# Performance work log

Hardware: AMD Instinct MI355X
Metric: run time of the kernel (lower is better)

The kernel has to match this reference:

```python
import jax, jax.numpy as jnp
import numpy as np
from jax import lax

B, T, P, H, O = 64, 96, 256, 128, 24  # batch, seq_len, num_points, hidden_dim, pred_len


def setup_inputs() -> dict:
    key = jax.random.key(0)
    ks = jax.random.split(key, 7)
    s = 1.0 / np.sqrt(H)  # torch LSTM/Linear default init scale
    return {
        "x": jax.random.normal(ks[0], (B, T, P, 1), dtype=jnp.float32),
        "W_ih": jax.random.uniform(ks[1], (P, 4 * H, 1), jnp.float32, -s, s),
        "W_hh": jax.random.uniform(ks[2], (P, 4 * H, H), jnp.float32, -s, s),
        "b_ih": jax.random.uniform(ks[3], (P, 4 * H), jnp.float32, -s, s),
        "b_hh": jax.random.uniform(ks[4], (P, 4 * H), jnp.float32, -s, s),
        "W_fc": jax.random.uniform(ks[5], (P, O, H), jnp.float32, -s, s),
        "b_fc": jax.random.uniform(ks[6], (P, O), jnp.float32, -s, s),
    }


def reference(x, W_ih, W_hh, b_ih, b_hh, W_fc, b_fc):
    # x: [B, T, P, F]; model uses only feature 0
    xs = x[..., 0]  # [B, T, P]
    # input_dim == 1, so input-to-gate contribution is a scaled broadcast of W_ih
    # precompute for all timesteps: [T, B, P, 4H]
    gx = jnp.einsum("btp,pg->tbpg", xs, W_ih[:, :, 0]) + (b_ih + b_hh)

    def step(carry, gxt):
        h, c = carry  # [B, P, H] each
        gates = gxt + jnp.einsum("bph,pgh->bpg", h, W_hh)  # [B, P, 4H]
        i, f, g, o = jnp.split(gates, 4, axis=-1)  # torch gate order i,f,g,o
        i = jax.nn.sigmoid(i)
        f = jax.nn.sigmoid(f)
        g = jnp.tanh(g)
        o = jax.nn.sigmoid(o)
        c = f * c + i * g
        h = o * jnp.tanh(c)
        return (h, c), None

    h0 = jnp.zeros((B, P, H), dtype=x.dtype)
    (h, _), _ = lax.scan(step, (h0, h0), gx)
    # per-point Linear on final hidden state: [B, P, O]
    out = jnp.einsum("bph,poh->bpo", h, W_fc) + b_fc
    # original stacks point outputs on last dim -> [B, pred_len, P]
    return jnp.transpose(out, (0, 2, 1))
```

## Files before the change

kernel.cpp:

```cpp
#include <hip/hip_runtime.h>
#include <hip/hip_bf16.h>

#define Bdim 64
#define Tdim 96
#define Pdim 256
#define Hdim 128
#define Gdim 512
#define Odim 24
#define BH   32

typedef _Float16 f16x8 __attribute__((ext_vector_type(8)));
typedef float    f32x16 __attribute__((ext_vector_type(16)));
typedef float    f32x2  __attribute__((ext_vector_type(2)));

union H8 { uint4 u4; unsigned short s[8]; _Float16 h[8]; f16x8 v; };
union HS { _Float16 h; unsigned short s; };

__device__ __forceinline__ float exp2_fast(float x) {
#if __has_builtin(__builtin_amdgcn_exp2f)
    return __builtin_amdgcn_exp2f(x);
#else
    return __expf(x * 0.6931471805599453f);
#endif
}

__global__ __launch_bounds__(1024, 4)
void lstm_fused(const float* __restrict__ x,
                const float* __restrict__ W_ih,
                const float* __restrict__ W_hh,
                const float* __restrict__ b_ih,
                const float* __restrict__ b_hh,
                const float* __restrict__ W_fc,
                const float* __restrict__ b_fc,
                float* __restrict__ out)
{
    __shared__ alignas(16) unsigned short hb0[2][BH * Hdim];
    __shared__ alignas(16) unsigned short hb1[2][BH * Hdim];

    const int p   = blockIdx.x;
    const int tid = threadIdx.x;
    const int w   = tid >> 6;
    const int l31 = tid & 31;
    const int hi  = (tid >> 5) & 1;

    const float L1 = 1.4426950408889634f;
    const float L2 = 2.0f * L1;

    for (int i = tid; i < 2 * BH * Hdim; i += 1024) ((unsigned short*)hb0)[i] = 0;
    for (int i = tid; i < 2 * BH * Hdim; i += 1024) ((unsigned short*)hb1)[i] = 0;

    f16x8 afr[9];
    {
        const int rp   = w * 32 + l31;
        const int u    = l31 >> 2;
        const int kl   = ((u & 1) << 2) | (u >> 1);
        const int orow = ((rp & 3) << 7) | (w * 8 + kl);
        const float sc = ((rp & 3) == 2) ? L2 : L1;
        const float* rowp = W_hh + (size_t)p * Gdim * Hdim + (size_t)orow * Hdim;
        #pragma unroll
        for (int ks = 0; ks < 8; ++ks) {
            int k0 = ks * 16 + hi * 8;
            float4 va = *(const float4*)(rowp + k0);
            float4 vb = *(const float4*)(rowp + k0 + 4);
            H8 u8;
            u8.h[0] = (_Float16)(sc * va.x); u8.h[1] = (_Float16)(sc * va.y);
            u8.h[2] = (_Float16)(sc * va.z); u8.h[3] = (_Float16)(sc * va.w);
            u8.h[4] = (_Float16)(sc * vb.x); u8.h[5] = (_Float16)(sc * vb.y);
            u8.h[6] = (_Float16)(sc * vb.z); u8.h[7] = (_Float16)(sc * vb.w);
            afr[ks] = u8.v;
        }
        H8 u9;
        #pragma unroll
        for (int j = 0; j < 8; ++j) u9.s[j] = 0;
        if (hi == 0) {
            u9.h[0] = (_Float16)(sc * W_ih[(size_t)p * Gdim + orow]);
            u9.h[1] = (_Float16)(sc * (b_ih[(size_t)p * Gdim + orow] +
                                       b_hh[(size_t)p * Gdim + orow]));
        }
        afr[8] = u9.v;
    }

    auto ldh = [&](const unsigned short* hb, int ks) -> H8 {
        H8 r;
        int c   = ks * 2 + hi;
        int off = (l31 << 8) + ((c ^ (l31 & 15)) << 4);
        r.u4 = *(const uint4*)((const char*)hb + off);
        return r;
    };

    auto ep_pair = [&](const f32x16& a, int j, f32x2* cr) -> unsigned {
        f32x2 yi = {a[8 * j + 0], a[8 * j + 4]};
        f32x2 yf = {a[8 * j + 1], a[8 * j + 5]};
        f32x2 yg = {a[8 * j + 2], a[8 * j + 6]};
        f32x2 yo = {a[8 * j + 3], a[8 * j + 7]};
        f32x2 Ef = {exp2_fast(-yf.x), exp2_fast(-yf.y)};
        f32x2 Ei = {exp2_fast(-yi.x), exp2_fast(-yi.y)};
        f32x2 Eg = {exp2_fast(yg.x),  exp2_fast(yg.y)};
        f32x2 t1 = Ef + 1.0f;
        f32x2 t2 = Ei + 1.0f;
        f32x2 t3 = Eg + 1.0f;
        f32x2 t4 = Eg - 1.0f;
        f32x2 den = (t1 * t2) * t3;
        f32x2 num = (cr[j] * t2) * t3 + (L2 * t4) * t1;
        float D = den.x * den.y;
        float r = __builtin_amdgcn_rcpf(D);
        f32x2 inv = {r * den.y, r * den.x};
        f32x2 cn  = num * inv;
        cn.x = __builtin_amdgcn_fmed3f(cn.x, -30.0f, 30.0f);
        cn.y = __builtin_amdgcn_fmed3f(cn.y, -30.0f, 30.0f);
        cr[j] = cn;
        f32x2 Eo = {exp2_fast(-yo.x), exp2_fast(-yo.y)};
        f32x2 Ec = {exp2_fast(cn.x),  exp2_fast(cn.y)};
        f32x2 d2 = (Eo + 1.0f) * (Ec + 1.0f);
        float D2 = d2.x * d2.y;
        float r2 = __builtin_amdgcn_rcpf(D2);
        f32x2 j2 = {r2 * d2.y, r2 * d2.x};
        f32x2 hv = (Ec - 1.0f) * j2;
        HS ha; ha.h = (_Float16)hv.x;
        HS hc; hc.h = (_Float16)hv.y;
        return (unsigned)ha.s | ((unsigned)hc.s << 16);
    };

    auto ep_write = [&](unsigned lo, unsigned hi2, unsigned short* wb) {
        int base = (l31 << 7) + ((w ^ (l31 & 15)) << 3) + (hi << 2);
        uint2 v; v.x = lo; v.y = hi2;
        *(uint2*)(wb + base) = v;
    };

    auto phase = [&](const unsigned short* rb, unsigned short* wb,
                     f32x16& acc, const f32x16& ar, f32x2* cr, float xv,
                     bool doGemm, bool doEp) {
        if (doGemm) {
            f32x16 z;
            #pragma unroll
            for (int j = 0; j < 16; ++j) z[j] = 0.f;
            H8 bg;
            #pragma unroll
            for (int j = 0; j < 8; ++j) bg.s[j] = 0;
            if (hi == 0) { bg.h[0] = (_Float16)xv; bg.h[1] = (_Float16)1.0f; }
            acc = __builtin_amdgcn_mfma_f32_32x32x16_f16(afr[8], bg.v, z, 0, 0, 0);
            H8 f0 = ldh(rb, 0), f1 = ldh(rb, 1);
            H8 f2 = ldh(rb, 2), f3 = ldh(rb, 3);
            acc = __builtin_amdgcn_mfma_f32_32x32x16_f16(afr[0], f0.v, acc, 0, 0, 0);
            acc = __builtin_amdgcn_mfma_f32_32x32x16_f16(afr[1], f1.v, acc, 0, 0, 0);
            unsigned e0 = 0;
            if (doEp) e0 = ep_pair(ar, 0, cr);
            H8 f4 = ldh(rb, 4), f5 = ldh(rb, 5);
            acc = __builtin_amdgcn_mfma_f32_32x32x16_f16(afr[2], f2.v, acc, 0, 0, 0);
            acc = __builtin_amdgcn_mfma_f32_32x32x16_f16(afr[3], f3.v, acc, 0, 0, 0);
            if (doEp) { unsigned e1 = ep_pair(ar, 1, cr); ep_write(e0, e1, wb); }
            H8 f6 = ldh(rb, 6), f7 = ldh(rb, 7);
            acc = __builtin_amdgcn_mfma_f32_32x32x16_f16(afr[4], f4.v, acc, 0, 0, 0);
            acc = __builtin_amdgcn_mfma_f32_32x32x16_f16(afr[5], f5.v, acc, 0, 0, 0);
            acc = __builtin_amdgcn_mfma_f32_32x32x16_f16(afr[6], f6.v, acc, 0, 0, 0);
            acc = __builtin_amdgcn_mfma_f32_32x32x16_f16(afr[7], f7.v, acc, 0, 0, 0);
        } else if (doEp) {
            unsigned e0 = ep_pair(ar, 0, cr);
            unsigned e1 = ep_pair(ar, 1, cr);
            ep_write(e0, e1, wb);
        }
    };

    f32x2 cre0[2] = {f32x2{0.f, 0.f}, f32x2{0.f, 0.f}};
    f32x2 cre1[2] = {f32x2{0.f, 0.f}, f32x2{0.f, 0.f}};
    f32x16 acc0, acc1;
    #pragma unroll
    for (int j = 0; j < 16; ++j) { acc0[j] = 0.f; acc1[j] = 0.f; }

    const float* xp0 = x + (size_t)((0 * BH + l31) * Tdim) * Pdim + p;
    const float* xp1 = x + (size_t)((1 * BH + l31) * Tdim) * Pdim + p;
    float xv0 = xp0[0];
    float xv1 = xp1[0];

    __syncthreads();

    for (int t = 0; t < Tdim; ++t) {
        const int P  = t & 1;
        const int tn = (t + 1 < Tdim) ? (t + 1) : t;
        float xn0 = xp0[(size_t)tn * Pdim];
        float xn1 = xp1[(size_t)tn * Pdim];

        phase(hb0[P], hb0[P ^ 1], acc0, acc1, cre1, xv0, true, false);
        phase(hb1[P], hb0[P ^ 1], acc1, acc0, cre0, xv1, true, true);
        phase(hb1[P], hb1[P ^ 1], acc1, acc1, cre1, 0.f, false, true);

        __syncthreads();
        xv0 = xn0;
        xv1 = xn1;
    }

    const float* wfc = W_fc + (size_t)p * Odim * Hdim;
    const float* bfc = b_fc + (size_t)p * Odim;
    for (int i = tid; i < Bdim * Odim; i += 1024) {
        int o = i % Odim;
        int b = i / Odim;
        int bl = (b < BH) ? b : (b - BH);
        const unsigned short* hr = (b < BH) ? (hb0[0] + (bl << 7))
                                            : (hb1[0] + (bl << 7));
        float s = bfc[o];
        const float* wr = wfc + o * Hdim;
        #pragma unroll 8
        for (int k2 = 0; k2 < Hdim; ++k2) {
            int idx = (((k2 >> 3) ^ (bl & 15)) << 3) + (k2 & 7);
            HS s2; s2.s = hr[idx];
            s = __builtin_fmaf(wr[k2], (float)s2.h, s);
        }
        out[(size_t)b * Odim * Pdim + (size_t)o * Pdim + p] = s;
    }
}

extern "C" void kernel_launch(void* const* d_in, const int* in_sizes, int n_in,
                              void* d_out, int out_size, void* d_ws, size_t ws_size,
                              hipStream_t stream) {
    const float* x    = (const float*)d_in[0];
    const float* W_ih = (const float*)d_in[1];
    const float* W_hh = (const float*)d_in[2];
    const float* b_ih = (const float*)d_in[3];
    const float* b_hh = (const float*)d_in[4];
    const float* W_fc = (const float*)d_in[5];
    const float* b_fc = (const float*)d_in[6];
    float* out = (float*)d_out;

    lstm_fused<<<dim3(Pdim), dim3(1024), 0, stream>>>(x, W_ih, W_hh, b_ih, b_hh, W_fc, b_fc, out);
}
```

Measured before the change: 390.3 us.

## Interleave both batch-half MFMA chains, then run epilogues after the GEMM

Replaces the three-phase schedule, which overlapped one batch-half's gate epilogue with the other half's MFMA chain, with a single per-step block. That block interleaves two independent MFMA accumulation chains (acc0 and acc1) and then runs both epilogues. The goal is to hide MFMA dependency latency with two independent chains. In exchange, the transcendental epilogue work no longer overlaps the matrix instructions. The bias/input B-fragment is also packed with a single 32-bit write.

```diff
diff --git a/kernel.cpp b/kernel.cpp
--- a/kernel.cpp
+++ b/kernel.cpp
@@ -127,45 +127,8 @@
         *(uint2*)(wb + base) = v;
     };
 
-    auto phase = [&](const unsigned short* rb, unsigned short* wb,
-                     f32x16& acc, const f32x16& ar, f32x2* cr, float xv,
-                     bool doGemm, bool doEp) {
-        if (doGemm) {
-            f32x16 z;
-            #pragma unroll
-            for (int j = 0; j < 16; ++j) z[j] = 0.f;
-            H8 bg;
-            #pragma unroll
-            for (int j = 0; j < 8; ++j) bg.s[j] = 0;
-            if (hi == 0) { bg.h[0] = (_Float16)xv; bg.h[1] = (_Float16)1.0f; }
-            acc = __builtin_amdgcn_mfma_f32_32x32x16_f16(afr[8], bg.v, z, 0, 0, 0);
-            H8 f0 = ldh(rb, 0), f1 = ldh(rb, 1);
-            H8 f2 = ldh(rb, 2), f3 = ldh(rb, 3);
-            acc = __builtin_amdgcn_mfma_f32_32x32x16_f16(afr[0], f0.v, acc, 0, 0, 0);
-            acc = __builtin_amdgcn_mfma_f32_32x32x16_f16(afr[1], f1.v, acc, 0, 0, 0);
-            unsigned e0 = 0;
-            if (doEp) e0 = ep_pair(ar, 0, cr);
-            H8 f4 = ldh(rb, 4), f5 = ldh(rb, 5);
-            acc = __builtin_amdgcn_mfma_f32_32x32x16_f16(afr[2], f2.v, acc, 0, 0, 0);
-            acc = __builtin_amdgcn_mfma_f32_32x32x16_f16(afr[3], f3.v, acc, 0, 0, 0);
-            if (doEp) { unsigned e1 = ep_pair(ar, 1, cr); ep_write(e0, e1, wb); }
-            H8 f6 = ldh(rb, 6), f7 = ldh(rb, 7);
-            acc = __builtin_amdgcn_mfma_f32_32x32x16_f16(afr[4], f4.v, acc, 0, 0, 0);
-            acc = __builtin_amdgcn_mfma_f32_32x32x16_f16(afr[5], f5.v, acc, 0, 0, 0);
-            acc = __builtin_amdgcn_mfma_f32_32x32x16_f16(afr[6], f6.v, acc, 0, 0, 0);
-            acc = __builtin_amdgcn_mfma_f32_32x32x16_f16(afr[7], f7.v, acc, 0, 0, 0);
-        } else if (doEp) {
-            unsigned e0 = ep_pair(ar, 0, cr);
-            unsigned e1 = ep_pair(ar, 1, cr);
-            ep_write(e0, e1, wb);
-        }
-    };
-
     f32x2 cre0[2] = {f32x2{0.f, 0.f}, f32x2{0.f, 0.f}};
     f32x2 cre1[2] = {f32x2{0.f, 0.f}, f32x2{0.f, 0.f}};
-    f32x16 acc0, acc1;
-    #pragma unroll
-    for (int j = 0; j < 16; ++j) { acc0[j] = 0.f; acc1[j] = 0.f; }
 
     const float* xp0 = x + (size_t)((0 * BH + l31) * Tdim) * Pdim + p;
     const float* xp1 = x + (size_t)((1 * BH + l31) * Tdim) * Pdim + p;
@@ -176,13 +139,64 @@
 
     for (int t = 0; t < Tdim; ++t) {
         const int P  = t & 1;
+        const unsigned short* rb0 = hb0[P];
+        const unsigned short* rb1 = hb1[P];
+        unsigned short* wbuf0 = hb0[P ^ 1];
+        unsigned short* wbuf1 = hb1[P ^ 1];
         const int tn = (t + 1 < Tdim) ? (t + 1) : t;
         float xn0 = xp0[(size_t)tn * Pdim];
         float xn1 = xp1[(size_t)tn * Pdim];
 
-        phase(hb0[P], hb0[P ^ 1], acc0, acc1, cre1, xv0, true, false);
-        phase(hb1[P], hb0[P ^ 1], acc1, acc0, cre0, xv1, true, true);
-        phase(hb1[P], hb1[P ^ 1], acc1, acc1, cre1, 0.f, false, true);
+        f32x16 acc0, acc1;
+        {
+            f32x16 z;
+            #pragma unroll
+            for (int j = 0; j < 16; ++j) z[j] = 0.f;
+            H8 bg0, bg1;
+            #pragma unroll
+            for (int j = 0; j < 8; ++j) { bg0.s[j] = 0; bg1.s[j] = 0; }
+            if (hi == 0) {
+                HS b0x; b0x.h = (_Float16)xv0;
+                HS b1x; b1x.h = (_Float16)xv1;
+                bg0.u4.x = (unsigned)b0x.s | (0x3C00u << 16);
+                bg1.u4.x = (unsigned)b1x.s | (0x3C00u << 16);
+            }
+            acc0 = __builtin_amdgcn_mfma_f32_32x32x16_f16(afr[8], bg0.v, z, 0, 0, 0);
+            acc1 = __builtin_amdgcn_mfma_f32_32x32x16_f16(afr[8], bg1.v, z, 0, 0, 0);
+            H8 a0 = ldh(rb0, 0), b0 = ldh(rb1, 0);
+            H8 a1 = ldh(rb0, 1), b1 = ldh(rb1, 1);
+            acc0 = __builtin_amdgcn_mfma_f32_32x32x16_f16(afr[0], a0.v, acc0, 0, 0, 0);
+            acc1 = __builtin_amdgcn_mfma_f32_32x32x16_f16(afr[0], b0.v, acc1, 0, 0, 0);
+            H8 a2 = ldh(rb0, 2), b2 = ldh(rb1, 2);
+            acc0 = __builtin_amdgcn_mfma_f32_32x32x16_f16(afr[1], a1.v, acc0, 0, 0, 0);
+            acc1 = __builtin_amdgcn_mfma_f32_32x32x16_f16(afr[1], b1.v, acc1, 0, 0, 0);
+            H8 a3 = ldh(rb0, 3), b3 = ldh(rb1, 3);
+            acc0 = __builtin_amdgcn_mfma_f32_32x32x16_f16(afr[2], a2.v, acc0, 0, 0, 0);
+            acc1 = __builtin_amdgcn_mfma_f32_32x32x16_f16(afr[2], b2.v, acc1, 0, 0, 0);
+            H8 a4 = ldh(rb0, 4), b4 = ldh(rb1, 4);
+            acc0 = __builtin_amdgcn_mfma_f32_32x32x16_f16(afr[3], a3.v, acc0, 0, 0, 0);
+            acc1 = __builtin_amdgcn_mfma_f32_32x32x16_f16(afr[3], b3.v, acc1, 0, 0, 0);
+            H8 a5 = ldh(rb0, 5), b5 = ldh(rb1, 5);
+            acc0 = __builtin_amdgcn_mfma_f32_32x32x16_f16(afr[4], a4.v, acc0, 0, 0, 0);
+            acc1 = __builtin_amdgcn_mfma_f32_32x32x16_f16(afr[4], b4.v, acc1, 0, 0, 0);
+            H8 a6 = ldh(rb0, 6), b6 = ldh(rb1, 6);
+            acc0 = __builtin_amdgcn_mfma_f32_32x32x16_f16(afr[5], a5.v, acc0, 0, 0, 0);
+            acc1 = __builtin_amdgcn_mfma_f32_32x32x16_f16(afr[5], b5.v, acc1, 0, 0, 0);
+            H8 a7 = ldh(rb0, 7), b7 = ldh(rb1, 7);
+            acc0 = __builtin_amdgcn_mfma_f32_32x32x16_f16(afr[6], a6.v, acc0, 0, 0, 0);
+            acc1 = __builtin_amdgcn_mfma_f32_32x32x16_f16(afr[6], b6.v, acc1, 0, 0, 0);
+            acc0 = __builtin_amdgcn_mfma_f32_32x32x16_f16(afr[7], a7.v, acc0, 0, 0, 0);
+            acc1 = __builtin_amdgcn_mfma_f32_32x32x16_f16(afr[7], b7.v, acc1, 0, 0, 0);
+        }
+
+        {
+            unsigned e00 = ep_pair(acc0, 0, cre0);
+            unsigned e01 = ep_pair(acc0, 1, cre0);
+            ep_write(e00, e01, wbuf0);
+            unsigned e10 = ep_pair(acc1, 0, cre1);
+            unsigned e11 = ep_pair(acc1, 1, cre1);
+            ep_write(e10, e11, wbuf1);
+        }
 
         __syncthreads();
         xv0 = xn0;
```

After: 385.5 us. About the same (-1.2%).
